# Optimization experiments

Measured on AMD Instinct MI355X. Metric: run time of the kernel, lower is better.

The kernel has to match this reference:

```python
import jax, jax.numpy as jnp
import numpy as np

B, T, K, H = 4, 2048, 128, 8
MASK = True


def setup_inputs() -> dict:
    key = jax.random.key(0)
    ks = jax.random.split(key, 6)
    s = 0.02
    return {
        "x": jax.random.normal(ks[0], (B, T, K), dtype=jnp.float32),
        "Wq": jax.random.normal(ks[1], (K, H * K), dtype=jnp.float32) * s,
        "Wk": jax.random.normal(ks[2], (K, H * K), dtype=jnp.float32) * s,
        "Wv": jax.random.normal(ks[3], (K, H * K), dtype=jnp.float32) * s,
        "Wu": jax.random.normal(ks[4], (H * K, K), dtype=jnp.float32) * s,
        "bu": jnp.zeros((K,), dtype=jnp.float32),
    }


def reference(x, Wq, Wk, Wv, Wu, bu):
    b, t, k = x.shape
    h = H
    q = (x @ Wq).reshape(b, t, h, k)
    kk = (x @ Wk).reshape(b, t, h, k)
    # module pre-scales values by k**-0.25 (idiosyncratic but faithful)
    v = (x @ Wv).reshape(b, t, h, k) * (k ** -0.25)
    # scores [b, h, t, t], scaled by k**-0.5
    scores = jnp.einsum('bthd,bshd->bhts', q, kk) * (k ** -0.5)
    if MASK:
        causal = jnp.tril(jnp.ones((t, t), dtype=bool))
        scores = jnp.where(causal, scores, -jnp.inf)
    w = jax.nn.softmax(scores, axis=-1)
    out = jnp.einsum('bhts,bshd->bthd', w, v).reshape(b, t, h * k)
    return out @ Wu + bu
```

## Files before the change

kernel.cpp:

```cpp
#include <hip/hip_runtime.h>
#include <hip/hip_bf16.h>
#include <math.h>

#define B_ 4
#define T_ 2048
#define D_ 128
#define H_ 8
#define BT_ 8192
#define HD_ 1024

typedef __attribute__((ext_vector_type(8))) short bf16x8;
typedef __attribute__((ext_vector_type(4))) float f32x4;

__device__ __forceinline__ short f2bf(float f) {
  union { float f; unsigned u; } v; v.f = f;
  return (short)((v.u + 0x8000u) >> 16);
}

#if __has_builtin(__builtin_amdgcn_exp2f)
#define EXP2F(x) __builtin_amdgcn_exp2f(x)
#else
#define EXP2F(x) exp2f(x)
#endif

#define QSCALE 0.12752040242046492f
#define VSCALE 0.29730177875068026f

__device__ __forceinline__ void gld16(const short* g, short* l) {
  __builtin_amdgcn_global_load_lds(
      (const __attribute__((address_space(1))) void*)g,
      (__attribute__((address_space(3))) void*)l, 16, 0, 0);
}

__device__ __forceinline__ void wu_transpose_body(
    const float* __restrict__ Wu, short* __restrict__ WuT,
    short* Tt, int kc, int tid)
{
  #pragma unroll 4
  for (int i = tid; i < 4096; i += 256) {
    int kl = i >> 5, n4 = (i & 31) << 2;
    float4 v = *(const float4*)&Wu[(size_t)(kc*128 + kl) * D_ + n4];
    float vv[4] = {v.x, v.y, v.z, v.w};
    #pragma unroll
    for (int j = 0; j < 4; j++) {
      int n = n4 + j;
      Tt[n*128 + (((kl >> 3) ^ (n & 15)) << 3) + (kl & 7)] = f2bf(vv[j]);
    }
  }
  __syncthreads();
  short* dst = WuT + (size_t)kc * 16384;
  #pragma unroll 2
  for (int i = tid; i < 2048; i += 256)
    *(bf16x8*)&dst[i*8] = *(bf16x8*)&Tt[i*8];
}

__global__ __launch_bounds__(256) void prep(
    const float* __restrict__ x, const float* __restrict__ Wq,
    const float* __restrict__ Wk, const float* __restrict__ Wv,
    const float* __restrict__ Wu,
    short* __restrict__ xbf, short* __restrict__ WT, short* __restrict__ WuT)
{
  __shared__ __align__(16) short Tt[128*128];
  const int tid = threadIdx.x;
  const int id = blockIdx.x;
  if (id < 24) {
    const int wsel = id >> 3, nt = id & 7;
    const float* W = (wsel == 0) ? Wq : (wsel == 1) ? Wk : Wv;
    #pragma unroll 4
    for (int i = tid; i < 4096; i += 256) {
      int k = i >> 5, n4 = (i & 31) << 2;
      float4 v = *(const float4*)&W[(size_t)k * HD_ + nt*128 + n4];
      float vv[4] = {v.x, v.y, v.z, v.w};
      #pragma unroll
      for (int j = 0; j < 4; j++) {
        int n = n4 + j;
        Tt[n*128 + (((k >> 3) ^ (n & 15)) << 3) + (k & 7)] = f2bf(vv[j]);
      }
    }
    __syncthreads();
    short* dst = WT + (size_t)id * 16384;
    #pragma unroll 2
    for (int i = tid; i < 2048; i += 256)
      *(bf16x8*)&dst[i*8] = *(bf16x8*)&Tt[i*8];
  } else if (id < 88) {
    const int xb = id - 24;
    const float* xs = x + (size_t)xb * 16384;
    short* dst = xbf + (size_t)xb * 16384;
    #pragma unroll 4
    for (int i = tid; i < 4096; i += 256) {
      float4 v = ((const float4*)xs)[i];
      int row = i >> 5, c = (i & 31) >> 1, half = i & 1;
      short4 p;
      p.x = f2bf(v.x); p.y = f2bf(v.y); p.z = f2bf(v.z); p.w = f2bf(v.w);
      *(short4*)&dst[(row*16 + (c ^ (row & 15)))*8 + half*4] = p;
    }
  } else {
    wu_transpose_body(Wu, WuT, Tt, id - 88, tid);
  }
}

__global__ __launch_bounds__(256, 2) void qkv_proj(
    const short* __restrict__ xbf, const short* __restrict__ WT,
    short* __restrict__ Qw, short* __restrict__ Kw, short* __restrict__ Vw)
{
  __shared__ __align__(16) short As[16384];
  __shared__ __align__(16) short Bs[16384];
  const int tid = threadIdx.x;
  const int w = tid >> 6, lane = tid & 63, quad = lane >> 4, l16 = lane & 15;
  const int m0 = (int)blockIdx.x * 128;
  const int head = (int)blockIdx.y;
  const int so = w*4096 + lane*8;

  {
    const short* asrc = xbf + (size_t)blockIdx.x * 16384;
    const short* bsrc = WT + (size_t)head * 16384;
    #pragma unroll
    for (int cc = 0; cc < 8; cc++) {
      gld16(asrc + so + cc*512, &As[w*4096 + cc*512]);
      gld16(bsrc + so + cc*512, &Bs[w*4096 + cc*512]);
    }
  }

  const int rA0 = (w & 1) * 64, rB0 = (w >> 1) * 64;
  const int b = m0 >> 11, t0g = m0 & 2047;
  const int h = head;

  #pragma unroll 1
  for (int wsel = 0; wsel < 3; wsel++) {
    __syncthreads();
    const short* RA = (wsel <= 1) ? Bs : As;
    const short* RB = (wsel <= 1) ? As : Bs;

    f32x4 acc[4][4];
    #pragma unroll
    for (int a = 0; a < 4; a++)
      #pragma unroll
      for (int bb = 0; bb < 4; bb++) acc[a][bb] = (f32x4){0.f, 0.f, 0.f, 0.f};

    #pragma unroll
    for (int kk = 0; kk < 4; kk++) {
      const int swz = ((kk*4 + quad) ^ l16) << 3;
      bf16x8 af[4], bfv[4];
      #pragma unroll
      for (int ai = 0; ai < 4; ai++) af[ai]  = *(const bf16x8*)&RA[(rA0 + ai*16 + l16)*128 + swz];
      #pragma unroll
      for (int bi = 0; bi < 4; bi++) bfv[bi] = *(const bf16x8*)&RB[(rB0 + bi*16 + l16)*128 + swz];
      #pragma unroll
      for (int ai = 0; ai < 4; ai++)
        #pragma unroll
        for (int bi = 0; bi < 4; bi++)
          acc[ai][bi] = __builtin_amdgcn_mfma_f32_16x16x32_bf16(af[ai], bfv[bi], acc[ai][bi], 0, 0, 0);
    }

    __syncthreads();
    if (wsel <= 1) {
      const float sc = wsel ? 1.0f : QSCALE;
      #pragma unroll
      for (int ai = 0; ai < 4; ai++) {
        #pragma unroll
        for (int bi = 0; bi < 4; bi++) {
          const int d0 = rA0 + ai*16 + quad*4;
          const int t  = rB0 + bi*16 + l16;
          const int tile = t >> 6, tl = t & 63;
          short4 p;
          p.x = f2bf(acc[ai][bi][0] * sc);
          p.y = f2bf(acc[ai][bi][1] * sc);
          p.z = f2bf(acc[ai][bi][2] * sc);
          p.w = f2bf(acc[ai][bi][3] * sc);
          *(short4*)&Bs[tile*8192 + tl*128 + (((d0 >> 3) ^ (tl & 15)) << 3) + (d0 & 7)] = p;
        }
      }
    } else {
      #pragma unroll
      for (int ai = 0; ai < 4; ai++) {
        #pragma unroll
        for (int bi = 0; bi < 4; bi++) {
          const int t0 = rA0 + ai*16 + quad*4;
          const int d  = rB0 + bi*16 + l16;
          const int tile = t0 >> 6, tl0 = t0 & 63;
          short4 p;
          p.x = f2bf(acc[ai][bi][0] * VSCALE);
          p.y = f2bf(acc[ai][bi][1] * VSCALE);
          p.z = f2bf(acc[ai][bi][2] * VSCALE);
          p.w = f2bf(acc[ai][bi][3] * VSCALE);
          *(short4*)&Bs[tile*8192 + d*64 + (((tl0 >> 3) ^ (d & 7)) << 3) + (tl0 & 7)] = p;
        }
      }
    }
    __syncthreads();

    short* base = ((wsel == 0) ? Qw : (wsel == 1) ? Kw : Vw)
                + (size_t)(b*H_ + h)*262144 + (size_t)t0g*128;
    #pragma unroll 2
    for (int i = tid; i < 2048; i += 256)
      *(bf16x8*)&base[i*8] = *(bf16x8*)&Bs[i*8];

    if (wsel < 2) {
      __syncthreads();
      const short* bsrc = WT + (size_t)((wsel + 1)*8 + head) * 16384;
      #pragma unroll
      for (int cc = 0; cc < 8; cc++)
        gld16(bsrc + so + cc*512, &Bs[w*4096 + cc*512]);
    }
  }
}

__global__ __launch_bounds__(256, 4) void attn_kernel(
    const short* __restrict__ Qw, const short* __restrict__ Kw,
    const short* __restrict__ Vw, short* __restrict__ attnw)
{
  __shared__ __align__(16) short Ks[8192];
  __shared__ __align__(16) short Vs[8192];
  __shared__ __align__(16) short Ps[4096];

  const int tid = threadIdx.x;
  const int id = (int)blockIdx.x;
  const int xcd = id & 7;
  const int j   = id >> 3;
  const int u   = j & 3;
  const int q   = (j >> 2) & 7;
  const int vv  = (j >> 5) & 3;
  const int slot = u ^ vv;
  const int qi = (slot == 0) ? q : (slot == 1) ? 15 - q
               : (slot == 2) ? 16 + q : 31 - q;
  const int bh = xcd | (u << 3);
  const int b = bh >> 3, h = bh & 7;
  const int w = tid >> 6, lane = tid & 63, quad = lane >> 4, l16 = lane & 15;
  const int rowQ = qi*64 + w*16;

  const short* Qp = Qw + (size_t)bh * 262144;
  const short* Kp = Kw + (size_t)bh * 262144;
  const short* Vp = Vw + (size_t)bh * 262144;

  bf16x8 qa[4];
  {
    const int tl = (rowQ & 63) + l16;
    const short* qp = Qp + ((size_t)(rowQ >> 6) << 13) + tl*128;
    #pragma unroll
    for (int kk = 0; kk < 4; kk++)
      qa[kk] = *(const bf16x8*)(qp + (((kk*4 + quad) ^ (tl & 15)) << 3));
  }

  f32x4 o[8];
  #pragma unroll
  for (int e = 0; e < 8; e++) o[e] = (f32x4){0,0,0,0};
  float l[4] = {0,0,0,0};

  short* Pw = &Ps[w*1024];
  const int so = w*2048 + lane*8;
  const int nIter = qi + 1;

  for (int it = 0; it < nIter; ++it) {
    if (it) __syncthreads();
    {
      const short* kt = Kp + ((size_t)it << 13);
      const short* vt = Vp + ((size_t)it << 13);
      #pragma unroll
      for (int cc = 0; cc < 4; cc++) {
        gld16(kt + so + cc*512, &Ks[w*2048 + cc*512]);
        gld16(vt + so + cc*512, &Vs[w*2048 + cc*512]);
      }
    }
    __syncthreads();

    f32x4 s[4];
    #pragma unroll
    for (int nj = 0; nj < 4; nj++) s[nj] = (f32x4){0,0,0,0};
    #pragma unroll
    for (int kk = 0; kk < 4; kk++) {
      const int swz = ((kk*4 + quad) ^ l16) << 3;
      #pragma unroll
      for (int nj = 0; nj < 4; nj++) {
        bf16x8 kb = *(const bf16x8*)&Ks[(nj*16 + l16)*128 + swz];
        s[nj] = __builtin_amdgcn_mfma_f32_16x16x32_bf16(qa[kk], kb, s[nj], 0, 0, 0);
      }
    }

    if (it < qi) {
      #pragma unroll
      for (int nj = 0; nj < 4; nj++) {
        #pragma unroll
        for (int r = 0; r < 4; r++) {
          float p = EXP2F(s[nj][r]);
          l[r] += p;
          const int row = quad*4 + r, col = nj*16 + l16;
          Pw[row*64 + (((col >> 3) ^ (row & 7)) << 3) + (col & 7)] = f2bf(p);
        }
      }
    } else {
      const int s0 = it * 64;
      #pragma unroll
      for (int nj = 0; nj < 4; nj++) {
        const int key = s0 + nj*16 + l16;
        #pragma unroll
        for (int r = 0; r < 4; r++) {
          float p = (key > rowQ + quad*4 + r) ? 0.f : EXP2F(s[nj][r]);
          l[r] += p;
          const int row = quad*4 + r, col = nj*16 + l16;
          Pw[row*64 + (((col >> 3) ^ (row & 7)) << 3) + (col & 7)] = f2bf(p);
        }
      }
    }

    #pragma unroll
    for (int kk2 = 0; kk2 < 2; kk2++) {
      const int swz = ((kk2*4 + quad) ^ (l16 & 7)) << 3;
      bf16x8 pa = *(bf16x8*)&Pw[l16*64 + swz];
      #pragma unroll
      for (int e = 0; e < 8; e++) {
        bf16x8 vb = *(const bf16x8*)&Vs[(e*16 + l16)*64 + swz];
        o[e] = __builtin_amdgcn_mfma_f32_16x16x32_bf16(pa, vb, o[e], 0, 0, 0);
      }
    }
  }

  #pragma unroll
  for (int r = 0; r < 4; r++) {
    float t = l[r];
    t += __shfl_xor(t, 1); t += __shfl_xor(t, 2);
    t += __shfl_xor(t, 4); t += __shfl_xor(t, 8);
    l[r] = 1.0f / t;
  }
  __syncthreads();
  #pragma unroll
  for (int e = 0; e < 8; e++) {
    const int c = e*2 + (l16 >> 3);
    #pragma unroll
    for (int r = 0; r < 4; r++) {
      const int lrow = w*16 + quad*4 + r;
      const int sub = lrow >> 5, r32 = lrow & 31;
      Ks[sub*4096 + r32*128 + ((c ^ (r32 & 15)) << 3) + (l16 & 7)] =
          f2bf(o[e][r] * l[r]);
    }
  }
  __syncthreads();
  const int st0 = b*64 + qi*2;
  #pragma unroll 2
  for (int i = tid; i < 1024; i += 256) {
    const int sub = i >> 9, rem = i & 511;
    short* dst = attnw + ((size_t)(st0 + sub)*8 + h)*4096 + rem*8;
    *(bf16x8*)dst = *(const bf16x8*)&Ks[i*8];
  }
}

__global__ __launch_bounds__(256) void wu_prep(
    const float* __restrict__ Wu, short* __restrict__ WuT)
{
  __shared__ __align__(16) short Tt[128*128];
  wu_transpose_body(Wu, WuT, Tt, blockIdx.x, threadIdx.x);
}

__global__ __launch_bounds__(256, 2) void out_proj(
    const short* __restrict__ attnw, const short* __restrict__ WuT,
    const float* __restrict__ bu, float* __restrict__ out)
{
  __shared__ __align__(16) short As2[2][2048];
  __shared__ __align__(16) short Bs2[2][16384];
  const int tid = threadIdx.x;
  const int w = tid >> 6, lane = tid & 63, quad = lane >> 4, l16 = lane & 15;
  const int m0 = (int)blockIdx.x * 16;
  const int mtile32 = m0 >> 5, half = (m0 >> 4) & 1;

  f32x4 o2[2];
  o2[0] = (f32x4){0,0,0,0}; o2[1] = (f32x4){0,0,0,0};

  {
    const short* ab = attnw + (size_t)(mtile32*8)*4096 + half*2048;
    gld16(ab + w*512 + lane*8, &As2[0][w*512]);
    #pragma unroll
    for (int cc = 0; cc < 8; cc++)
      gld16(WuT + w*4096 + cc*512 + lane*8, &Bs2[0][w*4096 + cc*512]);
  }
  int buf = 0;

  for (int kc = 0; kc < 8; kc++) {
    __syncthreads();
    if (kc < 7) {
      const short* ab = attnw + (size_t)(mtile32*8 + kc + 1)*4096 + half*2048;
      const short* bb = WuT + (size_t)(kc + 1)*16384;
      gld16(ab + w*512 + lane*8, &As2[buf^1][w*512]);
      #pragma unroll
      for (int cc = 0; cc < 8; cc++)
        gld16(bb + w*4096 + cc*512 + lane*8, &Bs2[buf^1][w*4096 + cc*512]);
    }
    const short* as = &As2[buf][0];
    const short* bs = &Bs2[buf][0];
    #pragma unroll
    for (int kk = 0; kk < 4; kk++) {
      const int swz = ((kk*4 + quad) ^ l16) << 3;
      bf16x8 a = *(const bf16x8*)&as[l16*128 + swz];
      #pragma unroll
      for (int e = 0; e < 2; e++) {
        bf16x8 bfr = *(const bf16x8*)&bs[((w*2 + e)*16 + l16)*128 + swz];
        o2[e] = __builtin_amdgcn_mfma_f32_16x16x32_bf16(a, bfr, o2[e], 0, 0, 0);
      }
    }
    buf ^= 1;
  }

  #pragma unroll
  for (int e = 0; e < 2; e++) {
    const int n = (w*2 + e)*16 + l16;
    const float bias = bu[n];
    #pragma unroll
    for (int r = 0; r < 4; r++) {
      const int mm = m0 + quad*4 + r;
      out[(size_t)mm*D_ + n] = o2[e][r] + bias;
    }
  }
}

extern "C" void kernel_launch(void* const* d_in, const int* in_sizes, int n_in,
                              void* d_out, int out_size, void* d_ws, size_t ws_size,
                              hipStream_t stream) {
  (void)in_sizes; (void)n_in; (void)out_size;
  const float* x  = (const float*)d_in[0];
  const float* Wq = (const float*)d_in[1];
  const float* Wk = (const float*)d_in[2];
  const float* Wv = (const float*)d_in[3];
  const float* Wu = (const float*)d_in[4];
  const float* bu = (const float*)d_in[5];
  float* out = (float*)d_out;

  const size_t headElems = (size_t)B_ * H_ * T_ * D_;
  short* Qw    = (short*)d_ws;
  short* Kw    = Qw + headElems;
  short* Vw    = Kw + headElems;
  short* attnw = Vw + headElems;
  short* xbf = attnw;
  short* WT  = attnw + 1048576;

  const bool extraWu = ws_size >= (64ull << 20) + (1ull << 20);
  short* WuT = extraWu ? (short*)((char*)d_ws + (64ull << 20)) : Kw;

  prep<<<dim3(extraWu ? 96 : 88), 256, 0, stream>>>(x, Wq, Wk, Wv, Wu, xbf, WT, WuT);
  qkv_proj<<<dim3(64, 8), 256, 0, stream>>>(xbf, WT, Qw, Kw, Vw);
  attn_kernel<<<dim3(1024), 256, 0, stream>>>(Qw, Kw, Vw, attnw);
  if (!extraWu) wu_prep<<<dim3(8), 256, 0, stream>>>(Wu, WuT);
  out_proj<<<dim3(512), 256, 0, stream>>>(attnw, WuT, bu, out);
}
```

Measured before the change: 151.6 us.

## Double-buffer K/V tiles with 32-key steps and prefetch next tile

The attention loop now processes 32 keys per iteration instead of 64 and splits the existing K and V shared buffers into two halves, so the next tile's global-to-LDS load is issued before the current tile is computed. The projection kernel now writes V in a 32-row tiled layout with a new swizzle to match. P storage is halved, and s_setprio is raised around the MFMA sections to favour matrix work. This removes one barrier per iteration and hides load latency, at the cost of twice as many loop iterations and smaller MFMA batches per sync.

```diff
diff --git a/kernel.cpp b/kernel.cpp
--- a/kernel.cpp
+++ b/kernel.cpp
@@ -177,13 +177,13 @@
         for (int bi = 0; bi < 4; bi++) {
           const int t0 = rA0 + ai*16 + quad*4;
           const int d  = rB0 + bi*16 + l16;
-          const int tile = t0 >> 6, tl0 = t0 & 63;
+          const int tile = t0 >> 5, tl0 = t0 & 31;
           short4 p;
           p.x = f2bf(acc[ai][bi][0] * VSCALE);
           p.y = f2bf(acc[ai][bi][1] * VSCALE);
           p.z = f2bf(acc[ai][bi][2] * VSCALE);
           p.w = f2bf(acc[ai][bi][3] * VSCALE);
-          *(short4*)&Bs[tile*8192 + d*64 + (((tl0 >> 3) ^ (d & 7)) << 3) + (tl0 & 7)] = p;
+          *(short4*)&Bs[tile*4096 + d*32 + ((((tl0 >> 3) ^ ((d >> 1) & 3)) << 3)) + (tl0 & 7)] = p;
         }
       }
     }
@@ -211,7 +211,7 @@
 {
   __shared__ __align__(16) short Ks[8192];
   __shared__ __align__(16) short Vs[8192];
-  __shared__ __align__(16) short Ps[4096];
+  __shared__ __align__(16) short Ps[2048];
 
   const int tid = threadIdx.x;
   const int id = (int)blockIdx.x;
@@ -246,72 +246,86 @@
   for (int e = 0; e < 8; e++) o[e] = (f32x4){0,0,0,0};
   float l[4] = {0,0,0,0};
 
-  short* Pw = &Ps[w*1024];
-  const int so = w*2048 + lane*8;
-  const int nIter = qi + 1;
+  short* Pw = &Ps[w*512];
+  const int stg = w*512 + lane*8;
+  const int nIter = 2*qi + 2;
+
+  {
+    #pragma unroll
+    for (int cc = 0; cc < 2; cc++) {
+      gld16(Kp + cc*2048 + stg, &Ks[cc*2048 + w*512]);
+      gld16(Vp + cc*2048 + stg, &Vs[cc*2048 + w*512]);
+    }
+  }
+
+  const int pswz = (quad ^ ((l16 >> 1) & 3)) << 3;
 
   for (int it = 0; it < nIter; ++it) {
-    if (it) __syncthreads();
-    {
-      const short* kt = Kp + ((size_t)it << 13);
-      const short* vt = Vp + ((size_t)it << 13);
-      #pragma unroll
-      for (int cc = 0; cc < 4; cc++) {
-        gld16(kt + so + cc*512, &Ks[w*2048 + cc*512]);
-        gld16(vt + so + cc*512, &Vs[w*2048 + cc*512]);
-      }
-    }
-    __syncthreads();
-
-    f32x4 s[4];
-    #pragma unroll
-    for (int nj = 0; nj < 4; nj++) s[nj] = (f32x4){0,0,0,0};
+    const int cur = (it & 1) << 12;
+    __syncthreads();
+
+    if (it + 1 < nIter) {
+      const int tt = it + 1;
+      const short* ksrc = Kp + (((size_t)(tt >> 1)) << 13) + (size_t)(tt & 1)*4096;
+      const short* vsrc = Vp + ((size_t)tt << 12);
+      const int nxt = cur ^ 4096;
+      #pragma unroll
+      for (int cc = 0; cc < 2; cc++) {
+        gld16(ksrc + cc*2048 + stg, &Ks[nxt + cc*2048 + w*512]);
+        gld16(vsrc + cc*2048 + stg, &Vs[nxt + cc*2048 + w*512]);
+      }
+    }
+
+    f32x4 s[2];
+    s[0] = (f32x4){0,0,0,0}; s[1] = (f32x4){0,0,0,0};
+    __builtin_amdgcn_s_setprio(1);
     #pragma unroll
     for (int kk = 0; kk < 4; kk++) {
       const int swz = ((kk*4 + quad) ^ l16) << 3;
       #pragma unroll
-      for (int nj = 0; nj < 4; nj++) {
-        bf16x8 kb = *(const bf16x8*)&Ks[(nj*16 + l16)*128 + swz];
+      for (int nj = 0; nj < 2; nj++) {
+        bf16x8 kb = *(const bf16x8*)&Ks[cur + (nj*16 + l16)*128 + swz];
         s[nj] = __builtin_amdgcn_mfma_f32_16x16x32_bf16(qa[kk], kb, s[nj], 0, 0, 0);
       }
     }
-
-    if (it < qi) {
-      #pragma unroll
-      for (int nj = 0; nj < 4; nj++) {
+    __builtin_amdgcn_s_setprio(0);
+
+    if (it < 2*qi) {
+      #pragma unroll
+      for (int nj = 0; nj < 2; nj++) {
         #pragma unroll
         for (int r = 0; r < 4; r++) {
           float p = EXP2F(s[nj][r]);
           l[r] += p;
           const int row = quad*4 + r, col = nj*16 + l16;
-          Pw[row*64 + (((col >> 3) ^ (row & 7)) << 3) + (col & 7)] = f2bf(p);
+          Pw[row*32 + ((((col >> 3) ^ ((row >> 1) & 3)) << 3)) + (col & 7)] = f2bf(p);
         }
       }
     } else {
-      const int s0 = it * 64;
-      #pragma unroll
-      for (int nj = 0; nj < 4; nj++) {
+      const int s0 = it * 32;
+      #pragma unroll
+      for (int nj = 0; nj < 2; nj++) {
         const int key = s0 + nj*16 + l16;
         #pragma unroll
         for (int r = 0; r < 4; r++) {
           float p = (key > rowQ + quad*4 + r) ? 0.f : EXP2F(s[nj][r]);
           l[r] += p;
           const int row = quad*4 + r, col = nj*16 + l16;
-          Pw[row*64 + (((col >> 3) ^ (row & 7)) << 3) + (col & 7)] = f2bf(p);
+          Pw[row*32 + ((((col >> 3) ^ ((row >> 1) & 3)) << 3)) + (col & 7)] = f2bf(p);
         }
       }
     }
 
-    #pragma unroll
-    for (int kk2 = 0; kk2 < 2; kk2++) {
-      const int swz = ((kk2*4 + quad) ^ (l16 & 7)) << 3;
-      bf16x8 pa = *(bf16x8*)&Pw[l16*64 + swz];
+    __builtin_amdgcn_s_setprio(1);
+    {
+      bf16x8 pa = *(bf16x8*)&Pw[l16*32 + pswz];
       #pragma unroll
       for (int e = 0; e < 8; e++) {
-        bf16x8 vb = *(const bf16x8*)&Vs[(e*16 + l16)*64 + swz];
+        bf16x8 vb = *(const bf16x8*)&Vs[cur + (e*16 + l16)*32 + pswz];
         o[e] = __builtin_amdgcn_mfma_f32_16x16x32_bf16(pa, vb, o[e], 0, 0, 0);
       }
     }
+    __builtin_amdgcn_s_setprio(0);
   }
 
   #pragma unroll
```

New measurement: 161.0 us. +6.2%, slower.

## Process two query tiles per attention block to reuse K/V loads

Applied to the files above, without the earlier changes.

Each attention block now handles two consecutive 64-row query tiles (128 rows), so every K/V tile loaded into shared memory feeds twice as many MFMAs. The grid is halved to 512 blocks with a paired causal balancing scheme (qt and 23-qt). Occupancy is lowered to 2 blocks per CU because registers and the P buffer double. The MFMA sections are wrapped in s_setprio raises. The trade-off is fewer blocks and lower occupancy to hide latency, plus one extra fully masked-style tile of work per block on the diagonal.

```diff
diff --git a/kernel.cpp b/kernel.cpp
--- a/kernel.cpp
+++ b/kernel.cpp
@@ -205,50 +205,50 @@
   }
 }
 
-__global__ __launch_bounds__(256, 4) void attn_kernel(
+__global__ __launch_bounds__(256, 2) void attn_kernel(
     const short* __restrict__ Qw, const short* __restrict__ Kw,
     const short* __restrict__ Vw, short* __restrict__ attnw)
 {
   __shared__ __align__(16) short Ks[8192];
   __shared__ __align__(16) short Vs[8192];
-  __shared__ __align__(16) short Ps[4096];
+  __shared__ __align__(16) short Ps[8192];
 
   const int tid = threadIdx.x;
   const int id = (int)blockIdx.x;
   const int xcd = id & 7;
   const int j   = id >> 3;
   const int u   = j & 3;
-  const int q   = (j >> 2) & 7;
-  const int vv  = (j >> 5) & 3;
-  const int slot = u ^ vv;
-  const int qi = (slot == 0) ? q : (slot == 1) ? 15 - q
-               : (slot == 2) ? 16 + q : 31 - q;
+  const int q   = j >> 2;
+  const int qt  = (q < 8) ? q : 23 - q;
   const int bh = xcd | (u << 3);
   const int b = bh >> 3, h = bh & 7;
   const int w = tid >> 6, lane = tid & 63, quad = lane >> 4, l16 = lane & 15;
-  const int rowQ = qi*64 + w*16;
 
   const short* Qp = Qw + (size_t)bh * 262144;
   const short* Kp = Kw + (size_t)bh * 262144;
   const short* Vp = Vw + (size_t)bh * 262144;
 
-  bf16x8 qa[4];
+  bf16x8 qa[2][4];
   {
-    const int tl = (rowQ & 63) + l16;
-    const short* qp = Qp + ((size_t)(rowQ >> 6) << 13) + tl*128;
-    #pragma unroll
-    for (int kk = 0; kk < 4; kk++)
-      qa[kk] = *(const bf16x8*)(qp + (((kk*4 + quad) ^ (tl & 15)) << 3));
-  }
-
-  f32x4 o[8];
+    const int tl = w*16 + l16;
+    #pragma unroll
+    for (int f = 0; f < 2; f++) {
+      const short* qp = Qp + (((size_t)(qt*2 + f)) << 13) + tl*128;
+      #pragma unroll
+      for (int kk = 0; kk < 4; kk++)
+        qa[f][kk] = *(const bf16x8*)(qp + (((kk*4 + quad) ^ l16) << 3));
+    }
+  }
+
+  f32x4 o[2][8];
   #pragma unroll
-  for (int e = 0; e < 8; e++) o[e] = (f32x4){0,0,0,0};
-  float l[4] = {0,0,0,0};
-
-  short* Pw = &Ps[w*1024];
+  for (int f = 0; f < 2; f++)
+    #pragma unroll
+    for (int e = 0; e < 8; e++) o[f][e] = (f32x4){0,0,0,0};
+  float l[2][4] = {{0,0,0,0},{0,0,0,0}};
+
   const int so = w*2048 + lane*8;
-  const int nIter = qi + 1;
+  const int nIter = 2*qt + 2;
 
   for (int it = 0; it < nIter; ++it) {
     if (it) __syncthreads();
@@ -263,83 +263,106 @@
     }
     __syncthreads();
 
-    f32x4 s[4];
-    #pragma unroll
-    for (int nj = 0; nj < 4; nj++) s[nj] = (f32x4){0,0,0,0};
+    f32x4 s[2][4];
+    #pragma unroll
+    for (int f = 0; f < 2; f++)
+      #pragma unroll
+      for (int nj = 0; nj < 4; nj++) s[f][nj] = (f32x4){0,0,0,0};
+
+    __builtin_amdgcn_s_setprio(1);
     #pragma unroll
     for (int kk = 0; kk < 4; kk++) {
       const int swz = ((kk*4 + quad) ^ l16) << 3;
       #pragma unroll
       for (int nj = 0; nj < 4; nj++) {
         bf16x8 kb = *(const bf16x8*)&Ks[(nj*16 + l16)*128 + swz];
-        s[nj] = __builtin_amdgcn_mfma_f32_16x16x32_bf16(qa[kk], kb, s[nj], 0, 0, 0);
-      }
-    }
-
-    if (it < qi) {
-      #pragma unroll
-      for (int nj = 0; nj < 4; nj++) {
+        s[0][nj] = __builtin_amdgcn_mfma_f32_16x16x32_bf16(qa[0][kk], kb, s[0][nj], 0, 0, 0);
+        s[1][nj] = __builtin_amdgcn_mfma_f32_16x16x32_bf16(qa[1][kk], kb, s[1][nj], 0, 0, 0);
+      }
+    }
+    __builtin_amdgcn_s_setprio(0);
+
+    #pragma unroll
+    for (int f = 0; f < 2; f++) {
+      short* Pw = &Ps[w*2048 + f*1024];
+      if (it < 2*qt + f) {
         #pragma unroll
-        for (int r = 0; r < 4; r++) {
-          float p = EXP2F(s[nj][r]);
-          l[r] += p;
-          const int row = quad*4 + r, col = nj*16 + l16;
-          Pw[row*64 + (((col >> 3) ^ (row & 7)) << 3) + (col & 7)] = f2bf(p);
+        for (int nj = 0; nj < 4; nj++) {
+          #pragma unroll
+          for (int r = 0; r < 4; r++) {
+            float p = EXP2F(s[f][nj][r]);
+            l[f][r] += p;
+            const int row = quad*4 + r, col = nj*16 + l16;
+            Pw[row*64 + (((col >> 3) ^ (row & 7)) << 3) + (col & 7)] = f2bf(p);
+          }
         }
-      }
-    } else {
-      const int s0 = it * 64;
-      #pragma unroll
-      for (int nj = 0; nj < 4; nj++) {
-        const int key = s0 + nj*16 + l16;
+      } else {
+        const int s0 = it * 64;
+        const int rowg = qt*128 + f*64 + w*16 + quad*4;
         #pragma unroll
-        for (int r = 0; r < 4; r++) {
-          float p = (key > rowQ + quad*4 + r) ? 0.f : EXP2F(s[nj][r]);
-          l[r] += p;
-          const int row = quad*4 + r, col = nj*16 + l16;
-          Pw[row*64 + (((col >> 3) ^ (row & 7)) << 3) + (col & 7)] = f2bf(p);
+        for (int nj = 0; nj < 4; nj++) {
+          const int key = s0 + nj*16 + l16;
+          #pragma unroll
+          for (int r = 0; r < 4; r++) {
+            float p = (key > rowg + r) ? 0.f : EXP2F(s[f][nj][r]);
+            l[f][r] += p;
+            const int row = quad*4 + r, col = nj*16 + l16;
+            Pw[row*64 + (((col >> 3) ^ (row & 7)) << 3) + (col & 7)] = f2bf(p);
+          }
         }
       }
     }
 
+    __builtin_amdgcn_s_setprio(1);
     #pragma unroll
     for (int kk2 = 0; kk2 < 2; kk2++) {
       const int swz = ((kk2*4 + quad) ^ (l16 & 7)) << 3;
-      bf16x8 pa = *(bf16x8*)&Pw[l16*64 + swz];
+      bf16x8 pa0 = *(bf16x8*)&Ps[w*2048 + l16*64 + swz];
+      bf16x8 pa1 = *(bf16x8*)&Ps[w*2048 + 1024 + l16*64 + swz];
       #pragma unroll
       for (int e = 0; e < 8; e++) {
         bf16x8 vb = *(const bf16x8*)&Vs[(e*16 + l16)*64 + swz];
-        o[e] = __builtin_amdgcn_mfma_f32_16x16x32_bf16(pa, vb, o[e], 0, 0, 0);
-      }
-    }
+        o[0][e] = __builtin_amdgcn_mfma_f32_16x16x32_bf16(pa0, vb, o[0][e], 0, 0, 0);
+        o[1][e] = __builtin_amdgcn_mfma_f32_16x16x32_bf16(pa1, vb, o[1][e], 0, 0, 0);
+      }
+    }
+    __builtin_amdgcn_s_setprio(0);
   }
 
   #pragma unroll
-  for (int r = 0; r < 4; r++) {
-    float t = l[r];
-    t += __shfl_xor(t, 1); t += __shfl_xor(t, 2);
-    t += __shfl_xor(t, 4); t += __shfl_xor(t, 8);
-    l[r] = 1.0f / t;
-  }
+  for (int f = 0; f < 2; f++)
+    #pragma unroll
+    for (int r = 0; r < 4; r++) {
+      float t = l[f][r];
+      t += __shfl_xor(t, 1); t += __shfl_xor(t, 2);
+      t += __shfl_xor(t, 4); t += __shfl_xor(t, 8);
+      l[f][r] = 1.0f / t;
+    }
   __syncthreads();
   #pragma unroll
-  for (int e = 0; e < 8; e++) {
-    const int c = e*2 + (l16 >> 3);
-    #pragma unroll
-    for (int r = 0; r < 4; r++) {
-      const int lrow = w*16 + quad*4 + r;
-      const int sub = lrow >> 5, r32 = lrow & 31;
-      Ks[sub*4096 + r32*128 + ((c ^ (r32 & 15)) << 3) + (l16 & 7)] =
-          f2bf(o[e][r] * l[r]);
+  for (int f = 0; f < 2; f++) {
+    short* img = f ? Vs : Ks;
+    #pragma unroll
+    for (int e = 0; e < 8; e++) {
+      const int c = e*2 + (l16 >> 3);
+      #pragma unroll
+      for (int r = 0; r < 4; r++) {
+        const int lrow = w*16 + quad*4 + r;
+        const int sub = lrow >> 5, r32 = lrow & 31;
+        img[sub*4096 + r32*128 + ((c ^ (r32 & 15)) << 3) + (l16 & 7)] =
+            f2bf(o[f][e][r] * l[f][r]);
+      }
     }
   }
   __syncthreads();
-  const int st0 = b*64 + qi*2;
+  const int st0 = b*64 + qt*4;
   #pragma unroll 2
-  for (int i = tid; i < 1024; i += 256) {
-    const int sub = i >> 9, rem = i & 511;
-    short* dst = attnw + ((size_t)(st0 + sub)*8 + h)*4096 + rem*8;
-    *(bf16x8*)dst = *(const bf16x8*)&Ks[i*8];
+  for (int i = tid; i < 2048; i += 256) {
+    const int f = i >> 10, k10 = i & 1023;
+    const int sub = k10 >> 9, rem = k10 & 511;
+    const short* src = f ? Vs : Ks;
+    short* dst = attnw + ((size_t)(st0 + f*2 + sub)*8 + h)*4096 + rem*8;
+    *(bf16x8*)dst = *(const bf16x8*)&src[k10*8];
   }
 }
 
@@ -435,7 +458,7 @@
 
   prep<<<dim3(extraWu ? 96 : 88), 256, 0, stream>>>(x, Wq, Wk, Wv, Wu, xbf, WT, WuT);
   qkv_proj<<<dim3(64, 8), 256, 0, stream>>>(xbf, WT, Qw, Kw, Vw);
-  attn_kernel<<<dim3(1024), 256, 0, stream>>>(Qw, Kw, Vw, attnw);
+  attn_kernel<<<dim3(512), 256, 0, stream>>>(Qw, Kw, Vw, attnw);
   if (!extraWu) wu_prep<<<dim3(8), 256, 0, stream>>>(Wu, WuT);
   out_proj<<<dim3(512), 256, 0, stream>>>(attnw, WuT, bu, out);
 }
```

New measurement: 161.7 us. +6.6%, slower.

## Switch attention kernel to 32x32x16 MFMA with 2x2 wave tiling

Applied to the files above, without the earlier changes.

The attention kernel moves from 16x16x32 MFMAs, where each wave owned 16 query rows, to 32x32x16 MFMAs over a 2x2 wave grid. Each wave now computes a 32x32 block of scores and a 32x64 slice of the output. Because each P row is now spread across two waves, the P tile is shared in LDS and needs an extra barrier, and the softmax row sums are combined across waves through LDS. The aim is fewer LDS fragment loads per MFMA and larger, more efficient matrix instructions, with s_setprio raised around the MFMA loops. The cost is one extra block-wide sync per iteration plus the cross-wave normalization.

```diff
diff --git a/kernel.cpp b/kernel.cpp
--- a/kernel.cpp
+++ b/kernel.cpp
@@ -11,6 +11,7 @@
 
 typedef __attribute__((ext_vector_type(8))) short bf16x8;
 typedef __attribute__((ext_vector_type(4))) float f32x4;
+typedef __attribute__((ext_vector_type(16))) float f32x16;
 
 __device__ __forceinline__ short f2bf(float f) {
   union { float f; unsigned u; } v; v.f = f;
@@ -225,30 +226,33 @@
                : (slot == 2) ? 16 + q : 31 - q;
   const int bh = xcd | (u << 3);
   const int b = bh >> 3, h = bh & 7;
-  const int w = tid >> 6, lane = tid & 63, quad = lane >> 4, l16 = lane & 15;
-  const int rowQ = qi*64 + w*16;
+  const int w = tid >> 6, lane = tid & 63;
+  const int wr = w >> 1, wc = w & 1;
+  const int l32 = lane & 31, lhi = lane >> 5;
 
   const short* Qp = Qw + (size_t)bh * 262144;
   const short* Kp = Kw + (size_t)bh * 262144;
   const short* Vp = Vw + (size_t)bh * 262144;
 
-  bf16x8 qa[4];
+  bf16x8 qa[8];
   {
-    const int tl = (rowQ & 63) + l16;
-    const short* qp = Qp + ((size_t)(rowQ >> 6) << 13) + tl*128;
-    #pragma unroll
-    for (int kk = 0; kk < 4; kk++)
-      qa[kk] = *(const bf16x8*)(qp + (((kk*4 + quad) ^ (tl & 15)) << 3));
-  }
-
-  f32x4 o[8];
-  #pragma unroll
-  for (int e = 0; e < 8; e++) o[e] = (f32x4){0,0,0,0};
-  float l[4] = {0,0,0,0};
-
-  short* Pw = &Ps[w*1024];
+    const int tl = wr*32 + l32;
+    const short* qp = Qp + ((size_t)qi << 13) + tl*128;
+    #pragma unroll
+    for (int st = 0; st < 8; st++) {
+      const int g = st*2 + lhi;
+      qa[st] = *(const bf16x8*)(qp + ((g ^ (tl & 15)) << 3));
+    }
+  }
+
+  f32x16 o[2];
+  o[0] = (f32x16){0,0,0,0,0,0,0,0,0,0,0,0,0,0,0,0};
+  o[1] = (f32x16){0,0,0,0,0,0,0,0,0,0,0,0,0,0,0,0};
+  float la[16] = {};
+
   const int so = w*2048 + lane*8;
   const int nIter = qi + 1;
+  const int key = wc*32 + l32;
 
   for (int it = 0; it < nIter; ++it) {
     if (it) __syncthreads();
@@ -263,74 +267,81 @@
     }
     __syncthreads();
 
-    f32x4 s[4];
-    #pragma unroll
-    for (int nj = 0; nj < 4; nj++) s[nj] = (f32x4){0,0,0,0};
-    #pragma unroll
-    for (int kk = 0; kk < 4; kk++) {
-      const int swz = ((kk*4 + quad) ^ l16) << 3;
-      #pragma unroll
-      for (int nj = 0; nj < 4; nj++) {
-        bf16x8 kb = *(const bf16x8*)&Ks[(nj*16 + l16)*128 + swz];
-        s[nj] = __builtin_amdgcn_mfma_f32_16x16x32_bf16(qa[kk], kb, s[nj], 0, 0, 0);
-      }
-    }
+    f32x16 s = (f32x16){0,0,0,0,0,0,0,0,0,0,0,0,0,0,0,0};
+    __builtin_amdgcn_s_setprio(1);
+    #pragma unroll
+    for (int st = 0; st < 8; st++) {
+      const int g = st*2 + lhi;
+      bf16x8 kb = *(const bf16x8*)&Ks[key*128 + ((g ^ (key & 15)) << 3)];
+      s = __builtin_amdgcn_mfma_f32_32x32x16_bf16(qa[st], kb, s, 0, 0, 0);
+    }
+    __builtin_amdgcn_s_setprio(0);
 
     if (it < qi) {
       #pragma unroll
-      for (int nj = 0; nj < 4; nj++) {
-        #pragma unroll
-        for (int r = 0; r < 4; r++) {
-          float p = EXP2F(s[nj][r]);
-          l[r] += p;
-          const int row = quad*4 + r, col = nj*16 + l16;
-          Pw[row*64 + (((col >> 3) ^ (row & 7)) << 3) + (col & 7)] = f2bf(p);
-        }
+      for (int r = 0; r < 16; r++) {
+        const int rl = (r & 3) + ((r >> 2) << 3) + (lhi << 2);
+        const int row = wr*32 + rl;
+        float p = EXP2F(s[r]);
+        la[r] += p;
+        Ps[row*64 + ((((key >> 3) ^ (row & 7)) << 3)) + (key & 7)] = f2bf(p);
       }
     } else {
-      const int s0 = it * 64;
-      #pragma unroll
-      for (int nj = 0; nj < 4; nj++) {
-        const int key = s0 + nj*16 + l16;
-        #pragma unroll
-        for (int r = 0; r < 4; r++) {
-          float p = (key > rowQ + quad*4 + r) ? 0.f : EXP2F(s[nj][r]);
-          l[r] += p;
-          const int row = quad*4 + r, col = nj*16 + l16;
-          Pw[row*64 + (((col >> 3) ^ (row & 7)) << 3) + (col & 7)] = f2bf(p);
-        }
-      }
-    }
-
-    #pragma unroll
-    for (int kk2 = 0; kk2 < 2; kk2++) {
-      const int swz = ((kk2*4 + quad) ^ (l16 & 7)) << 3;
-      bf16x8 pa = *(bf16x8*)&Pw[l16*64 + swz];
-      #pragma unroll
-      for (int e = 0; e < 8; e++) {
-        bf16x8 vb = *(const bf16x8*)&Vs[(e*16 + l16)*64 + swz];
-        o[e] = __builtin_amdgcn_mfma_f32_16x16x32_bf16(pa, vb, o[e], 0, 0, 0);
-      }
-    }
+      #pragma unroll
+      for (int r = 0; r < 16; r++) {
+        const int rl = (r & 3) + ((r >> 2) << 3) + (lhi << 2);
+        const int row = wr*32 + rl;
+        float p = (key > row) ? 0.f : EXP2F(s[r]);
+        la[r] += p;
+        Ps[row*64 + ((((key >> 3) ^ (row & 7)) << 3)) + (key & 7)] = f2bf(p);
+      }
+    }
+    __syncthreads();
+
+    __builtin_amdgcn_s_setprio(1);
+    #pragma unroll
+    for (int st = 0; st < 4; st++) {
+      const int prow = wr*32 + l32;
+      const int kg = st*2 + lhi;
+      bf16x8 pa = *(const bf16x8*)&Ps[prow*64 + ((kg ^ (prow & 7)) << 3)];
+      #pragma unroll
+      for (int dt = 0; dt < 2; dt++) {
+        const int d = wc*64 + dt*32 + l32;
+        bf16x8 vb = *(const bf16x8*)&Vs[d*64 + ((kg ^ (d & 7)) << 3)];
+        o[dt] = __builtin_amdgcn_mfma_f32_32x32x16_bf16(pa, vb, o[dt], 0, 0, 0);
+      }
+    }
+    __builtin_amdgcn_s_setprio(0);
   }
 
   #pragma unroll
-  for (int r = 0; r < 4; r++) {
-    float t = l[r];
-    t += __shfl_xor(t, 1); t += __shfl_xor(t, 2);
-    t += __shfl_xor(t, 4); t += __shfl_xor(t, 8);
-    l[r] = 1.0f / t;
+  for (int r = 0; r < 16; r++) {
+    float t = la[r];
+    t += __shfl_xor(t, 1); t += __shfl_xor(t, 2); t += __shfl_xor(t, 4);
+    t += __shfl_xor(t, 8); t += __shfl_xor(t, 16);
+    la[r] = t;
+  }
+  __syncthreads();
+  float* Lr = (float*)Ps;
+  if (l32 == 0) {
+    #pragma unroll
+    for (int r = 0; r < 16; r++) {
+      const int rl = (r & 3) + ((r >> 2) << 3) + (lhi << 2);
+      Lr[wc*64 + wr*32 + rl] = la[r];
+    }
   }
   __syncthreads();
   #pragma unroll
-  for (int e = 0; e < 8; e++) {
-    const int c = e*2 + (l16 >> 3);
-    #pragma unroll
-    for (int r = 0; r < 4; r++) {
-      const int lrow = w*16 + quad*4 + r;
-      const int sub = lrow >> 5, r32 = lrow & 31;
-      Ks[sub*4096 + r32*128 + ((c ^ (r32 & 15)) << 3) + (l16 & 7)] =
-          f2bf(o[e][r] * l[r]);
+  for (int r = 0; r < 16; r++) {
+    const int rl = (r & 3) + ((r >> 2) << 3) + (lhi << 2);
+    const int row = wr*32 + rl;
+    const float inv = 1.0f / (Lr[row] + Lr[64 + row]);
+    #pragma unroll
+    for (int dt = 0; dt < 2; dt++) {
+      const int col = wc*64 + dt*32 + l32;
+      const int sub = row >> 5, r32 = row & 31, c = col >> 3;
+      Ks[sub*4096 + r32*128 + ((c ^ (r32 & 15)) << 3) + (col & 7)] =
+          f2bf(o[dt][r] * inv);
     }
   }
   __syncthreads();
```

Measured after the change: 240.0 us. 1.58x slower.
